# Optimization experiments

Hardware: AMD Instinct MI355X
Metric: run time of the kernel (lower is better)

Reference implementation:

```python
import jax, jax.numpy as jnp
import numpy as np

D = 384      # ViT-S feature dim (feat_dim_lookup['s'])
H = 6        # module forces num_heads = 6
L = 12       # ViT-S depth
RATIO = 0.1  # attention_mask_ratio
EPS = 1e-6


def layernorm(x, g, b):
    m = x.mean(-1, keepdims=True)
    v = ((x - m) ** 2).mean(-1, keepdims=True)
    return (x - m) * jax.lax.rsqrt(v + EPS) * g + b


def masked_attn(x, w_qkv, b_qkv, w_o, b_o):
    # Patch._fix_attn_masking: full softmax attention, threshold at ratio*row_max, renormalize.
    B, N, Dm = x.shape
    dh = Dm // H
    qkv = (x @ w_qkv + b_qkv).reshape(B, N, 3, H, dh)
    q = qkv[:, :, 0].transpose(0, 2, 1, 3)  # [B,H,N,dh]
    k = qkv[:, :, 1].transpose(0, 2, 1, 3)
    v = qkv[:, :, 2].transpose(0, 2, 1, 3)
    scores = jnp.einsum('bhqd,bhkd->bhqk', q, k) * (dh ** -0.5)
    attn = jax.nn.softmax(scores, axis=-1)
    thresh = RATIO * attn.max(axis=-1, keepdims=True)
    attn = jnp.where(attn >= thresh, attn, 0.0)
    attn = attn / attn.sum(axis=-1, keepdims=True)  # re-normalize
    out = jnp.einsum('bhqk,bhkd->bhqd', attn, v)
    out = out.transpose(0, 2, 1, 3).reshape(B, N, Dm)
    return out @ w_o + b_o, attn


def block(x, p):
    w_qkv, b_qkv, w_o, b_o, g1, be1, g2, be2, w1, b1, w2, b2 = p
    h, attn = masked_attn(layernorm(x, g1, be1), w_qkv, b_qkv, w_o, b_o)
    x = x + h
    h = layernorm(x, g2, be2) @ w1 + b1
    h = jax.nn.gelu(h, approximate=False) @ w2 + b2
    return x + h, attn


def setup_inputs() -> dict:
    key = jax.random.key(0)
    ks = jax.random.split(key, 8)
    B, N = 2, 962  # 2 transforms; (1+(160-8)//5)**2 + 1 cls = 962 tokens
    s = 0.02
    return {
        'x': jax.random.normal(ks[0], (B, N, D), jnp.float32),
        'w_qkv': jax.random.normal(ks[1], (L, D, 3 * D), jnp.float32) * s,
        'b_qkv': jnp.zeros((L, 3 * D), jnp.float32),
        'w_proj': jax.random.normal(ks[2], (L, D, D), jnp.float32) * s,
        'b_proj': jnp.zeros((L, D), jnp.float32),
        'ln1_g': jnp.ones((L, D), jnp.float32),
        'ln1_b': jnp.zeros((L, D), jnp.float32),
        'ln2_g': jnp.ones((L, D), jnp.float32),
        'ln2_b': jnp.zeros((L, D), jnp.float32),
        'w_fc1': jax.random.normal(ks[3], (L, D, 4 * D), jnp.float32) * s,
        'b_fc1': jnp.zeros((L, 4 * D), jnp.float32),
        'w_fc2': jax.random.normal(ks[4], (L, 4 * D, D), jnp.float32) * s,
        'b_fc2': jnp.zeros((L, D), jnp.float32),
        'lnf_g': jnp.ones((D,), jnp.float32),
        'lnf_b': jnp.zeros((D,), jnp.float32),
    }


def reference(x, w_qkv, b_qkv, w_proj, b_proj, ln1_g, ln1_b, ln2_g, ln2_b,
              w_fc1, b_fc1, w_fc2, b_fc2, lnf_g, lnf_b):
    params = (w_qkv, b_qkv, w_proj, b_proj, ln1_g, ln1_b, ln2_g, ln2_b,
              w_fc1, b_fc1, w_fc2, b_fc2)
    first = jax.tree_util.tree_map(lambda a: a[:-1], params)
    last = jax.tree_util.tree_map(lambda a: a[-1], params)

    def scan_fn(h, p):
        h, _ = block(h, p)
        return h, None

    x, _ = jax.lax.scan(scan_fn, x, first)  # blocks 0..L-2
    x, attn = block(x, last)                # last block, keep masked attention
    feats = layernorm(x, lnf_g, lnf_b)      # [B, N, D]
    return feats, attn
```

## Files before the change

kernel.cpp:

```cpp
#include <hip/hip_runtime.h>
#include <hip/hip_bf16.h>
#include <math.h>

typedef __bf16 bf16_t;
typedef __bf16 bf16x8 __attribute__((ext_vector_type(8)));
typedef float f32x4 __attribute__((ext_vector_type(4)));

#define NEGBIG -3.0e38f

__global__ void __launch_bounds__(256) tr_k(
    const float* __restrict__ W, bf16_t* __restrict__ Wt, int K, int N)
{
    __shared__ float T[32][33];
    const size_t per = (size_t)K * N;
    const float* Wl = W + blockIdx.z * per;
    bf16_t* Wtl = Wt + blockIdx.z * per;
    int n0 = blockIdx.x * 32, k0 = blockIdx.y * 32;
    int tx = threadIdx.x & 31, ty = threadIdx.x >> 5;
#pragma unroll
    for (int i = 0; i < 4; ++i)
        T[ty + 8 * i][tx] = Wl[(size_t)(k0 + ty + 8 * i) * N + n0 + tx];
    __syncthreads();
#pragma unroll
    for (int i = 0; i < 4; ++i)
        Wtl[(size_t)(n0 + ty + 8 * i) * K + k0 + tx] = (bf16_t)T[tx][ty + 8 * i];
}

template <int MODE>
__global__ void __launch_bounds__(256) gemm_k(
    const bf16_t* __restrict__ A, const bf16_t* __restrict__ Bt,
    const float* __restrict__ bias, int M, int N, int K,
    bf16_t* __restrict__ outb,
    bf16_t* __restrict__ qb, bf16_t* __restrict__ kb, bf16_t* __restrict__ vtb)
{
    __shared__ alignas(16) bf16_t As[2][64][72];
    __shared__ alignas(16) bf16_t Bs[2][64][72];

    const int tid  = threadIdx.x;
    const int wave = tid >> 6, lane = tid & 63;
    const int m0 = blockIdx.y * 64, n0 = blockIdx.x * 64;
    const int rb = (wave >> 1) * 32, cb = (wave & 1) * 32;
    const int q4 = lane >> 4, mm = lane & 15;

    const int lrow = tid >> 3;
    const int lcol = (tid & 7) * 8;

    const bf16_t* pA0 = A  + (size_t)(m0 + lrow) * K + lcol;
    const bf16_t* pA1 = pA0 + (size_t)32 * K;
    const bf16_t* pB0 = Bt + (size_t)(n0 + lrow) * K + lcol;
    const bf16_t* pB1 = pB0 + (size_t)32 * K;

    f32x4 acc[2][2] = {};
    bf16x8 va0, va1, vb0, vb1;

    va0 = *(const bf16x8*)(pA0);
    va1 = *(const bf16x8*)(pA1);
    vb0 = *(const bf16x8*)(pB0);
    vb1 = *(const bf16x8*)(pB1);
    *(bf16x8*)(&As[0][lrow][lcol])      = va0;
    *(bf16x8*)(&As[0][lrow + 32][lcol]) = va1;
    *(bf16x8*)(&Bs[0][lrow][lcol])      = vb0;
    *(bf16x8*)(&Bs[0][lrow + 32][lcol]) = vb1;

    int cur = 0;
    for (int k0 = 0; k0 < K; k0 += 64) {
        __syncthreads();
        const bool has_next = (k0 + 64 < K);
        if (has_next) {
            va0 = *(const bf16x8*)(pA0 + k0 + 64);
            va1 = *(const bf16x8*)(pA1 + k0 + 64);
            vb0 = *(const bf16x8*)(pB0 + k0 + 64);
            vb1 = *(const bf16x8*)(pB1 + k0 + 64);
        }
#pragma unroll
        for (int kc = 0; kc < 64; kc += 32) {
            bf16x8 a0 = *(const bf16x8*)(&As[cur][rb + mm][kc + q4 * 8]);
            bf16x8 a1 = *(const bf16x8*)(&As[cur][rb + 16 + mm][kc + q4 * 8]);
            bf16x8 b0 = *(const bf16x8*)(&Bs[cur][cb + mm][kc + q4 * 8]);
            bf16x8 b1 = *(const bf16x8*)(&Bs[cur][cb + 16 + mm][kc + q4 * 8]);
            acc[0][0] = __builtin_amdgcn_mfma_f32_16x16x32_bf16(a0, b0, acc[0][0], 0, 0, 0);
            acc[0][1] = __builtin_amdgcn_mfma_f32_16x16x32_bf16(a0, b1, acc[0][1], 0, 0, 0);
            acc[1][0] = __builtin_amdgcn_mfma_f32_16x16x32_bf16(a1, b0, acc[1][0], 0, 0, 0);
            acc[1][1] = __builtin_amdgcn_mfma_f32_16x16x32_bf16(a1, b1, acc[1][1], 0, 0, 0);
        }
        if (has_next) {
            int nxt = cur ^ 1;
            *(bf16x8*)(&As[nxt][lrow][lcol])      = va0;
            *(bf16x8*)(&As[nxt][lrow + 32][lcol]) = va1;
            *(bf16x8*)(&Bs[nxt][lrow][lcol])      = vb0;
            *(bf16x8*)(&Bs[nxt][lrow + 32][lcol]) = vb1;
            cur = nxt;
        }
    }

#pragma unroll
    for (int i = 0; i < 2; ++i)
#pragma unroll
    for (int j = 0; j < 2; ++j) {
        int gc = n0 + cb + j * 16 + mm;
        float bv = bias[gc];
#pragma unroll
        for (int r = 0; r < 4; ++r) {
            int gr = m0 + rb + i * 16 + q4 * 4 + r;
            if (gr >= M) continue;
            float val = acc[i][j][r] + bv;
            if (MODE == 2) {
                float g = 0.5f * val * (1.0f + erff(val * 0.70710678118654752f));
                outb[(size_t)gr * N + gc] = (bf16_t)g;
            } else {
                int which = gc / 384, rem = gc % 384;
                int h = rem >> 6, d = rem & 63;
                int b = gr / 962, n = gr % 962;
                int bh = b * 6 + h;
                bf16_t bvv = (bf16_t)val;
                if (which == 0)      qb[((size_t)bh * 962 + n) * 64 + d] = bvv;
                else if (which == 1) kb[((size_t)bh * 962 + n) * 64 + d] = bvv;
                else                 vtb[((size_t)bh * 64 + d) * 992 + n] = bvv;
            }
        }
    }
}

template <int KLEN>
__global__ void __launch_bounds__(256) gemm_sp(
    const bf16_t* __restrict__ A, int lda,
    const bf16_t* __restrict__ Bt, int ldb,
    const float* __restrict__ bias, int M, int N,
    float* __restrict__ resid)
{
    __shared__ alignas(16) bf16_t As[2][64][72];
    __shared__ alignas(16) bf16_t Bs[2][64][72];

    const int tid  = threadIdx.x;
    const int wave = tid >> 6, lane = tid & 63;
    const int m0 = blockIdx.y * 64, n0 = blockIdx.x * 64;
    const int rb = (wave >> 1) * 32, cb = (wave & 1) * 32;
    const int q4 = lane >> 4, mm = lane & 15;
    const int ks = blockIdx.z * KLEN;

    const int lrow = tid >> 3;
    const int lcol = (tid & 7) * 8;

    const bf16_t* pA0 = A  + (size_t)(m0 + lrow) * lda + ks + lcol;
    const bf16_t* pA1 = pA0 + (size_t)32 * lda;
    const bf16_t* pB0 = Bt + (size_t)(n0 + lrow) * ldb + ks + lcol;
    const bf16_t* pB1 = pB0 + (size_t)32 * ldb;

    f32x4 acc[2][2] = {};
    bf16x8 va0, va1, vb0, vb1;

    va0 = *(const bf16x8*)(pA0);
    va1 = *(const bf16x8*)(pA1);
    vb0 = *(const bf16x8*)(pB0);
    vb1 = *(const bf16x8*)(pB1);
    *(bf16x8*)(&As[0][lrow][lcol])      = va0;
    *(bf16x8*)(&As[0][lrow + 32][lcol]) = va1;
    *(bf16x8*)(&Bs[0][lrow][lcol])      = vb0;
    *(bf16x8*)(&Bs[0][lrow + 32][lcol]) = vb1;

    int cur = 0;
    for (int k0 = 0; k0 < KLEN; k0 += 64) {
        __syncthreads();
        const bool has_next = (k0 + 64 < KLEN);
        if (has_next) {
            va0 = *(const bf16x8*)(pA0 + k0 + 64);
            va1 = *(const bf16x8*)(pA1 + k0 + 64);
            vb0 = *(const bf16x8*)(pB0 + k0 + 64);
            vb1 = *(const bf16x8*)(pB1 + k0 + 64);
        }
#pragma unroll
        for (int kc = 0; kc < 64; kc += 32) {
            bf16x8 a0 = *(const bf16x8*)(&As[cur][rb + mm][kc + q4 * 8]);
            bf16x8 a1 = *(const bf16x8*)(&As[cur][rb + 16 + mm][kc + q4 * 8]);
            bf16x8 b0 = *(const bf16x8*)(&Bs[cur][cb + mm][kc + q4 * 8]);
            bf16x8 b1 = *(const bf16x8*)(&Bs[cur][cb + 16 + mm][kc + q4 * 8]);
            acc[0][0] = __builtin_amdgcn_mfma_f32_16x16x32_bf16(a0, b0, acc[0][0], 0, 0, 0);
            acc[0][1] = __builtin_amdgcn_mfma_f32_16x16x32_bf16(a0, b1, acc[0][1], 0, 0, 0);
            acc[1][0] = __builtin_amdgcn_mfma_f32_16x16x32_bf16(a1, b0, acc[1][0], 0, 0, 0);
            acc[1][1] = __builtin_amdgcn_mfma_f32_16x16x32_bf16(a1, b1, acc[1][1], 0, 0, 0);
        }
        if (has_next) {
            int nxt = cur ^ 1;
            *(bf16x8*)(&As[nxt][lrow][lcol])      = va0;
            *(bf16x8*)(&As[nxt][lrow + 32][lcol]) = va1;
            *(bf16x8*)(&Bs[nxt][lrow][lcol])      = vb0;
            *(bf16x8*)(&Bs[nxt][lrow + 32][lcol]) = vb1;
            cur = nxt;
        }
    }

#pragma unroll
    for (int i = 0; i < 2; ++i)
#pragma unroll
    for (int j = 0; j < 2; ++j) {
        int gc = n0 + cb + j * 16 + mm;
        float bv = (blockIdx.z == 0) ? bias[gc] : 0.f;
#pragma unroll
        for (int r = 0; r < 4; ++r) {
            int gr = m0 + rb + i * 16 + q4 * 4 + r;
            if (gr >= M) continue;
            atomicAdd(&resid[(size_t)gr * N + gc], acc[i][j][r] + bv);
        }
    }
}

__global__ void __launch_bounds__(256) attn_k(
    const bf16_t* __restrict__ qb, const bf16_t* __restrict__ kb,
    const bf16_t* __restrict__ vtb, bf16_t* __restrict__ attnout,
    float* __restrict__ attn_save)
{
    __shared__ alignas(16) bf16_t S[16][1000];

    const int tid  = threadIdx.x;
    const int wave = tid >> 6, lane = tid & 63;
    const int q4 = lane >> 4, mm = lane & 15;
    const int bh = blockIdx.y, qt = blockIdx.x;
    const int qrow0 = qt * 16;

    int qr = qrow0 + mm; if (qr > 961) qr = 961;
    const bf16_t* qptr = qb + ((size_t)bh * 962 + qr) * 64 + q4 * 8;
    bf16x8 aq0 = *(const bf16x8*)(qptr);
    bf16x8 aq1 = *(const bf16x8*)(qptr + 32);

    for (int ct = wave; ct < 61; ct += 4) {
        int kr = ct * 16 + mm; if (kr > 961) kr = 961;
        const bf16_t* kptr = kb + ((size_t)bh * 962 + kr) * 64 + q4 * 8;
        bf16x8 b0 = *(const bf16x8*)(kptr);
        bf16x8 b1 = *(const bf16x8*)(kptr + 32);
        f32x4 acc = {};
        acc = __builtin_amdgcn_mfma_f32_16x16x32_bf16(aq0, b0, acc, 0, 0, 0);
        acc = __builtin_amdgcn_mfma_f32_16x16x32_bf16(aq1, b1, acc, 0, 0, 0);
        int col = ct * 16 + mm;
#pragma unroll
        for (int r = 0; r < 4; ++r) {
            int row = q4 * 4 + r;
            if (col < 962) S[row][col] = (bf16_t)(acc[r] * 0.125f);
        }
    }
    for (int idx = tid; idx < 16 * 38; idx += 256) {
        int r = idx / 38, c = 962 + idx % 38;
        S[r][c] = (bf16_t)NEGBIG;
    }
    __syncthreads();

    const int trow = tid >> 4, ti = tid & 15;
    float e[8][8];
    float mx = NEGBIG;
#pragma unroll
    for (int t = 0; t < 8; ++t) {
        int c8 = ti * 8 + 128 * t;
        bf16x8 xv;
        if (c8 < 1000) xv = *(const bf16x8*)(&S[trow][c8]);
        else {
#pragma unroll
            for (int j = 0; j < 8; ++j) xv[j] = (bf16_t)NEGBIG;
        }
#pragma unroll
        for (int j = 0; j < 8; ++j) { e[t][j] = (float)xv[j]; mx = fmaxf(mx, e[t][j]); }
    }
#pragma unroll
    for (int off = 8; off > 0; off >>= 1) mx = fmaxf(mx, __shfl_xor(mx, off, 16));

    float sum = 0.f;
#pragma unroll
    for (int t = 0; t < 8; ++t)
#pragma unroll
    for (int j = 0; j < 8; ++j) {
        float ev = __expf(e[t][j] - mx);
        e[t][j] = ev;
        if (ev >= 0.1f) sum += ev;
    }
#pragma unroll
    for (int off = 8; off > 0; off >>= 1) sum += __shfl_xor(sum, off, 16);
    float inv = 1.0f / sum;

    int row_g = qrow0 + trow;
#pragma unroll
    for (int t = 0; t < 8; ++t) {
        int c8 = ti * 8 + 128 * t;
        if (c8 >= 1000) continue;
        bf16x8 pv;
#pragma unroll
        for (int j = 0; j < 8; ++j) {
            float pp = (e[t][j] >= 0.1f) ? e[t][j] * inv : 0.f;
            e[t][j] = pp;
            pv[j] = (bf16_t)pp;
        }
        *(bf16x8*)(&S[trow][c8]) = pv;
        if (attn_save && row_g < 962) {
#pragma unroll
            for (int j = 0; j < 8; ++j)
                if (c8 + j < 962)
                    attn_save[((size_t)bh * 962 + row_g) * 962 + c8 + j] = e[t][j];
        }
    }
    __syncthreads();

    const int wc0 = wave * 16;
    f32x4 o = {};
    for (int kc = 0; kc < 31; ++kc) {
        bf16x8 pa = *(const bf16x8*)(&S[mm][kc * 32 + q4 * 8]);
        bf16x8 vb = *(const bf16x8*)(vtb + ((size_t)bh * 64 + wc0 + mm) * 992 + kc * 32 + q4 * 8);
        o = __builtin_amdgcn_mfma_f32_16x16x32_bf16(pa, vb, o, 0, 0, 0);
    }
    int b = bh / 6, h = bh % 6;
#pragma unroll
    for (int r = 0; r < 4; ++r) {
        int qrr = qrow0 + q4 * 4 + r;
        if (qrr < 962)
            attnout[((size_t)(b * 962 + qrr)) * 384 + h * 64 + wc0 + mm] = (bf16_t)o[r];
    }
}

template <typename OT>
__global__ void __launch_bounds__(256) ln_k(
    const float* __restrict__ x, const float* __restrict__ g,
    const float* __restrict__ b, OT* __restrict__ out)
{
    int t = blockIdx.x * 4 + (threadIdx.x >> 6);
    int lane = threadIdx.x & 63;
    const float* xp = x + (size_t)t * 384;
    float v[6];
    float s = 0.f;
#pragma unroll
    for (int i = 0; i < 6; ++i) { v[i] = xp[lane + 64 * i]; s += v[i]; }
    for (int off = 32; off > 0; off >>= 1) s += __shfl_xor(s, off);
    float mean = s * (1.0f / 384.0f);
    float s2 = 0.f;
#pragma unroll
    for (int i = 0; i < 6; ++i) { float d = v[i] - mean; s2 += d * d; }
    for (int off = 32; off > 0; off >>= 1) s2 += __shfl_xor(s2, off);
    float rstd = rsqrtf(s2 * (1.0f / 384.0f) + 1e-6f);
#pragma unroll
    for (int i = 0; i < 6; ++i) {
        int c = lane + 64 * i;
        float y = (v[i] - mean) * rstd * g[c] + b[c];
        out[(size_t)t * 384 + c] = (OT)y;
    }
}

extern "C" void kernel_launch(void* const* d_in, const int* in_sizes, int n_in,
                              void* d_out, int out_size, void* d_ws, size_t ws_size,
                              hipStream_t stream)
{
    const float* xin    = (const float*)d_in[0];
    const float* w_qkv  = (const float*)d_in[1];
    const float* b_qkv  = (const float*)d_in[2];
    const float* w_proj = (const float*)d_in[3];
    const float* b_proj = (const float*)d_in[4];
    const float* ln1g   = (const float*)d_in[5];
    const float* ln1b   = (const float*)d_in[6];
    const float* ln2g   = (const float*)d_in[7];
    const float* ln2b   = (const float*)d_in[8];
    const float* w_fc1  = (const float*)d_in[9];
    const float* b_fc1  = (const float*)d_in[10];
    const float* w_fc2  = (const float*)d_in[11];
    const float* b_fc2  = (const float*)d_in[12];
    const float* lnfg   = (const float*)d_in[13];
    const float* lnfb   = (const float*)d_in[14];

    float* feats     = (float*)d_out;
    float* attn_save = feats + 738816;

    char* p = (char*)d_ws;
    auto alloc = [&](size_t bytes) {
        char* r = p;
        p += (bytes + 255) & ~(size_t)255;
        return r;
    };
    float*  x_f32   = (float*)alloc(1924ull * 384 * 4);
    bf16_t* xn      = (bf16_t*)alloc(1984ull * 384 * 2);
    bf16_t* qbuf    = (bf16_t*)alloc(12ull * 962 * 64 * 2);
    bf16_t* kbuf    = (bf16_t*)alloc(12ull * 962 * 64 * 2);
    bf16_t* vtbuf   = (bf16_t*)alloc(12ull * 64 * 992 * 2);
    bf16_t* attnout = (bf16_t*)alloc(1984ull * 384 * 2);
    bf16_t* mlp1    = (bf16_t*)alloc(1984ull * 1536 * 2);
    bf16_t* wt_qkv  = (bf16_t*)alloc(12ull * 1152 * 384 * 2);
    bf16_t* wt_proj = (bf16_t*)alloc(12ull * 384 * 384 * 2);
    bf16_t* wt_fc1  = (bf16_t*)alloc(12ull * 1536 * 384 * 2);
    bf16_t* wt_fc2  = (bf16_t*)alloc(12ull * 384 * 1536 * 2);

    tr_k<<<dim3(36, 12, 12), dim3(256), 0, stream>>>(w_qkv,  wt_qkv,  384, 1152);
    tr_k<<<dim3(12, 12, 12), dim3(256), 0, stream>>>(w_proj, wt_proj, 384, 384);
    tr_k<<<dim3(48, 12, 12), dim3(256), 0, stream>>>(w_fc1,  wt_fc1,  384, 1536);
    tr_k<<<dim3(12, 48, 12), dim3(256), 0, stream>>>(w_fc2,  wt_fc2,  1536, 384);

    hipMemcpyAsync(x_f32, xin, 738816ull * 4, hipMemcpyDeviceToDevice, stream);

    for (int l = 0; l < 12; ++l) {
        ln_k<bf16_t><<<dim3(481), dim3(256), 0, stream>>>(x_f32, ln1g + l * 384, ln1b + l * 384, xn);
        gemm_k<0><<<dim3(18, 31), dim3(256), 0, stream>>>(
            xn, wt_qkv + (size_t)l * 1152 * 384, b_qkv + l * 1152,
            1924, 1152, 384, nullptr, qbuf, kbuf, vtbuf);
        attn_k<<<dim3(61, 12), dim3(256), 0, stream>>>(
            qbuf, kbuf, vtbuf, attnout, (l == 11) ? attn_save : (float*)nullptr);
        gemm_sp<192><<<dim3(6, 31, 2), dim3(256), 0, stream>>>(
            attnout, 384, wt_proj + (size_t)l * 384 * 384, 384, b_proj + l * 384,
            1924, 384, x_f32);
        ln_k<bf16_t><<<dim3(481), dim3(256), 0, stream>>>(x_f32, ln2g + l * 384, ln2b + l * 384, xn);
        gemm_k<2><<<dim3(24, 31), dim3(256), 0, stream>>>(
            xn, wt_fc1 + (size_t)l * 1536 * 384, b_fc1 + l * 1536,
            1924, 1536, 384, mlp1, nullptr, nullptr, nullptr);
        gemm_sp<384><<<dim3(6, 31, 4), dim3(256), 0, stream>>>(
            mlp1, 1536, wt_fc2 + (size_t)l * 384 * 1536, 1536, b_fc2 + l * 384,
            1924, 384, x_f32);
    }
    ln_k<float><<<dim3(481), dim3(256), 0, stream>>>(x_f32, lnfg, lnfb, feats);
}
```

Measured before the change: 1.062 ms.

## Use direct global-to-LDS loads with XOR swizzle, merge transpose launches, add MFMA priority

```diff
diff --git a/kernel.cpp b/kernel.cpp
--- a/kernel.cpp
+++ b/kernel.cpp
@@ -8,14 +8,74 @@
 
 #define NEGBIG -3.0e38f
 
-__global__ void __launch_bounds__(256) tr_k(
-    const float* __restrict__ W, bf16_t* __restrict__ Wt, int K, int N)
+__device__ __forceinline__ void gload16(const void* g, void* l) {
+    __builtin_amdgcn_global_load_lds(
+        (const __attribute__((address_space(1))) void*)g,
+        (__attribute__((address_space(3))) void*)l, 16, 0, 0);
+}
+
+struct GemmSM { bf16_t As[2][64][64]; bf16_t Bs[2][64][64]; };
+
+__device__ __forceinline__ void gemm_core(
+    GemmSM* sg, const bf16_t* A, int lda, const bf16_t* Bt, int ldb, int K,
+    f32x4 acc[2][2])
+{
+    const int tid  = threadIdx.x;
+    const int wave = tid >> 6, lane = tid & 63;
+    const int rb = (wave >> 1) * 32, cb = (wave & 1) * 32;
+    const int q4 = lane >> 4, mm = lane & 15;
+    const int sw = (mm & 7) << 3;
+
+    const int sr   = lane >> 3;
+    const int scol = ((lane & 7) ^ sr) << 3;
+    const bf16_t* gA0 = A  + (size_t)(8 * wave + sr) * lda + scol;
+    const bf16_t* gA1 = gA0 + (size_t)32 * lda;
+    const bf16_t* gB0 = Bt + (size_t)(8 * wave + sr) * ldb + scol;
+    const bf16_t* gB1 = gB0 + (size_t)32 * ldb;
+
+    auto stage = [&](int buf, int k) {
+        gload16(gA0 + k, &sg->As[buf][8 * wave][0]);
+        gload16(gA1 + k, &sg->As[buf][8 * wave + 32][0]);
+        gload16(gB0 + k, &sg->Bs[buf][8 * wave][0]);
+        gload16(gB1 + k, &sg->Bs[buf][8 * wave + 32][0]);
+    };
+
+    stage(0, 0);
+    int cur = 0;
+    for (int k0 = 0; k0 < K; k0 += 64) {
+        __syncthreads();
+        if (k0 + 64 < K) stage(cur ^ 1, k0 + 64);
+#pragma unroll
+        for (int kc = 0; kc < 64; kc += 32) {
+            bf16x8 a0 = *(const bf16x8*)(&sg->As[cur][rb + mm][(kc + q4 * 8) ^ sw]);
+            bf16x8 a1 = *(const bf16x8*)(&sg->As[cur][rb + 16 + mm][(kc + q4 * 8) ^ sw]);
+            bf16x8 b0 = *(const bf16x8*)(&sg->Bs[cur][cb + mm][(kc + q4 * 8) ^ sw]);
+            bf16x8 b1 = *(const bf16x8*)(&sg->Bs[cur][cb + 16 + mm][(kc + q4 * 8) ^ sw]);
+            acc[0][0] = __builtin_amdgcn_mfma_f32_16x16x32_bf16(a0, b0, acc[0][0], 0, 0, 0);
+            acc[0][1] = __builtin_amdgcn_mfma_f32_16x16x32_bf16(a0, b1, acc[0][1], 0, 0, 0);
+            acc[1][0] = __builtin_amdgcn_mfma_f32_16x16x32_bf16(a1, b0, acc[1][0], 0, 0, 0);
+            acc[1][1] = __builtin_amdgcn_mfma_f32_16x16x32_bf16(a1, b1, acc[1][1], 0, 0, 0);
+        }
+        cur ^= 1;
+    }
+}
+
+__global__ void __launch_bounds__(256) trall_k(
+    const float* __restrict__ w_qkv, const float* __restrict__ w_proj,
+    const float* __restrict__ w_fc1, const float* __restrict__ w_fc2,
+    bf16_t* __restrict__ wt_qkv, bf16_t* __restrict__ wt_proj,
+    bf16_t* __restrict__ wt_fc1, bf16_t* __restrict__ wt_fc2)
 {
     __shared__ float T[32][33];
-    const size_t per = (size_t)K * N;
-    const float* Wl = W + blockIdx.z * per;
-    bf16_t* Wtl = Wt + blockIdx.z * per;
-    int n0 = blockIdx.x * 32, k0 = blockIdx.y * 32;
+    int t = blockIdx.x;
+    int z = t / 1728, r = t % 1728;
+    const float* W; bf16_t* Wt; int K, N, n0, k0;
+    if (r < 432)       { W = w_qkv;  Wt = wt_qkv;  K = 384;  N = 1152; n0 = (r % 36) * 32;               k0 = (r / 36) * 32; }
+    else if (r < 576)  { W = w_proj; Wt = wt_proj; K = 384;  N = 384;  int rr = r - 432;  n0 = (rr % 12) * 32; k0 = (rr / 12) * 32; }
+    else if (r < 1152) { W = w_fc1;  Wt = wt_fc1;  K = 384;  N = 1536; int rr = r - 576;  n0 = (rr % 48) * 32; k0 = (rr / 48) * 32; }
+    else               { W = w_fc2;  Wt = wt_fc2;  K = 1536; N = 384;  int rr = r - 1152; n0 = (rr % 12) * 32; k0 = (rr / 12) * 32; }
+    const float* Wl = W + (size_t)z * K * N;
+    bf16_t* Wtl = Wt + (size_t)z * K * N;
     int tx = threadIdx.x & 31, ty = threadIdx.x >> 5;
 #pragma unroll
     for (int i = 0; i < 4; ++i)
@@ -33,66 +93,14 @@
     bf16_t* __restrict__ outb,
     bf16_t* __restrict__ qb, bf16_t* __restrict__ kb, bf16_t* __restrict__ vtb)
 {
-    __shared__ alignas(16) bf16_t As[2][64][72];
-    __shared__ alignas(16) bf16_t Bs[2][64][72];
-
-    const int tid  = threadIdx.x;
+    __shared__ GemmSM sm;
+    const int tid = threadIdx.x;
     const int wave = tid >> 6, lane = tid & 63;
     const int m0 = blockIdx.y * 64, n0 = blockIdx.x * 64;
     const int rb = (wave >> 1) * 32, cb = (wave & 1) * 32;
     const int q4 = lane >> 4, mm = lane & 15;
-
-    const int lrow = tid >> 3;
-    const int lcol = (tid & 7) * 8;
-
-    const bf16_t* pA0 = A  + (size_t)(m0 + lrow) * K + lcol;
-    const bf16_t* pA1 = pA0 + (size_t)32 * K;
-    const bf16_t* pB0 = Bt + (size_t)(n0 + lrow) * K + lcol;
-    const bf16_t* pB1 = pB0 + (size_t)32 * K;
-
     f32x4 acc[2][2] = {};
-    bf16x8 va0, va1, vb0, vb1;
-
-    va0 = *(const bf16x8*)(pA0);
-    va1 = *(const bf16x8*)(pA1);
-    vb0 = *(const bf16x8*)(pB0);
-    vb1 = *(const bf16x8*)(pB1);
-    *(bf16x8*)(&As[0][lrow][lcol])      = va0;
-    *(bf16x8*)(&As[0][lrow + 32][lcol]) = va1;
-    *(bf16x8*)(&Bs[0][lrow][lcol])      = vb0;
-    *(bf16x8*)(&Bs[0][lrow + 32][lcol]) = vb1;
-
-    int cur = 0;
-    for (int k0 = 0; k0 < K; k0 += 64) {
-        __syncthreads();
-        const bool has_next = (k0 + 64 < K);
-        if (has_next) {
-            va0 = *(const bf16x8*)(pA0 + k0 + 64);
-            va1 = *(const bf16x8*)(pA1 + k0 + 64);
-            vb0 = *(const bf16x8*)(pB0 + k0 + 64);
-            vb1 = *(const bf16x8*)(pB1 + k0 + 64);
-        }
-#pragma unroll
-        for (int kc = 0; kc < 64; kc += 32) {
-            bf16x8 a0 = *(const bf16x8*)(&As[cur][rb + mm][kc + q4 * 8]);
-            bf16x8 a1 = *(const bf16x8*)(&As[cur][rb + 16 + mm][kc + q4 * 8]);
-            bf16x8 b0 = *(const bf16x8*)(&Bs[cur][cb + mm][kc + q4 * 8]);
-            bf16x8 b1 = *(const bf16x8*)(&Bs[cur][cb + 16 + mm][kc + q4 * 8]);
-            acc[0][0] = __builtin_amdgcn_mfma_f32_16x16x32_bf16(a0, b0, acc[0][0], 0, 0, 0);
-            acc[0][1] = __builtin_amdgcn_mfma_f32_16x16x32_bf16(a0, b1, acc[0][1], 0, 0, 0);
-            acc[1][0] = __builtin_amdgcn_mfma_f32_16x16x32_bf16(a1, b0, acc[1][0], 0, 0, 0);
-            acc[1][1] = __builtin_amdgcn_mfma_f32_16x16x32_bf16(a1, b1, acc[1][1], 0, 0, 0);
-        }
-        if (has_next) {
-            int nxt = cur ^ 1;
-            *(bf16x8*)(&As[nxt][lrow][lcol])      = va0;
-            *(bf16x8*)(&As[nxt][lrow + 32][lcol]) = va1;
-            *(bf16x8*)(&Bs[nxt][lrow][lcol])      = vb0;
-            *(bf16x8*)(&Bs[nxt][lrow + 32][lcol]) = vb1;
-            cur = nxt;
-        }
-    }
-
+    gemm_core(&sm, A + (size_t)m0 * K, K, Bt + (size_t)n0 * K, K, K, acc);
 #pragma unroll
     for (int i = 0; i < 2; ++i)
 #pragma unroll
@@ -128,67 +136,15 @@
     const float* __restrict__ bias, int M, int N,
     float* __restrict__ resid)
 {
-    __shared__ alignas(16) bf16_t As[2][64][72];
-    __shared__ alignas(16) bf16_t Bs[2][64][72];
-
-    const int tid  = threadIdx.x;
+    __shared__ GemmSM sm;
+    const int tid = threadIdx.x;
     const int wave = tid >> 6, lane = tid & 63;
     const int m0 = blockIdx.y * 64, n0 = blockIdx.x * 64;
     const int rb = (wave >> 1) * 32, cb = (wave & 1) * 32;
     const int q4 = lane >> 4, mm = lane & 15;
     const int ks = blockIdx.z * KLEN;
-
-    const int lrow = tid >> 3;
-    const int lcol = (tid & 7) * 8;
-
-    const bf16_t* pA0 = A  + (size_t)(m0 + lrow) * lda + ks + lcol;
-    const bf16_t* pA1 = pA0 + (size_t)32 * lda;
-    const bf16_t* pB0 = Bt + (size_t)(n0 + lrow) * ldb + ks + lcol;
-    const bf16_t* pB1 = pB0 + (size_t)32 * ldb;
-
     f32x4 acc[2][2] = {};
-    bf16x8 va0, va1, vb0, vb1;
-
-    va0 = *(const bf16x8*)(pA0);
-    va1 = *(const bf16x8*)(pA1);
-    vb0 = *(const bf16x8*)(pB0);
-    vb1 = *(const bf16x8*)(pB1);
-    *(bf16x8*)(&As[0][lrow][lcol])      = va0;
-    *(bf16x8*)(&As[0][lrow + 32][lcol]) = va1;
-    *(bf16x8*)(&Bs[0][lrow][lcol])      = vb0;
-    *(bf16x8*)(&Bs[0][lrow + 32][lcol]) = vb1;
-
-    int cur = 0;
-    for (int k0 = 0; k0 < KLEN; k0 += 64) {
-        __syncthreads();
-        const bool has_next = (k0 + 64 < KLEN);
-        if (has_next) {
-            va0 = *(const bf16x8*)(pA0 + k0 + 64);
-            va1 = *(const bf16x8*)(pA1 + k0 + 64);
-            vb0 = *(const bf16x8*)(pB0 + k0 + 64);
-            vb1 = *(const bf16x8*)(pB1 + k0 + 64);
-        }
-#pragma unroll
-        for (int kc = 0; kc < 64; kc += 32) {
-            bf16x8 a0 = *(const bf16x8*)(&As[cur][rb + mm][kc + q4 * 8]);
-            bf16x8 a1 = *(const bf16x8*)(&As[cur][rb + 16 + mm][kc + q4 * 8]);
-            bf16x8 b0 = *(const bf16x8*)(&Bs[cur][cb + mm][kc + q4 * 8]);
-            bf16x8 b1 = *(const bf16x8*)(&Bs[cur][cb + 16 + mm][kc + q4 * 8]);
-            acc[0][0] = __builtin_amdgcn_mfma_f32_16x16x32_bf16(a0, b0, acc[0][0], 0, 0, 0);
-            acc[0][1] = __builtin_amdgcn_mfma_f32_16x16x32_bf16(a0, b1, acc[0][1], 0, 0, 0);
-            acc[1][0] = __builtin_amdgcn_mfma_f32_16x16x32_bf16(a1, b0, acc[1][0], 0, 0, 0);
-            acc[1][1] = __builtin_amdgcn_mfma_f32_16x16x32_bf16(a1, b1, acc[1][1], 0, 0, 0);
-        }
-        if (has_next) {
-            int nxt = cur ^ 1;
-            *(bf16x8*)(&As[nxt][lrow][lcol])      = va0;
-            *(bf16x8*)(&As[nxt][lrow + 32][lcol]) = va1;
-            *(bf16x8*)(&Bs[nxt][lrow][lcol])      = vb0;
-            *(bf16x8*)(&Bs[nxt][lrow + 32][lcol]) = vb1;
-            cur = nxt;
-        }
-    }
-
+    gemm_core(&sm, A + (size_t)m0 * lda + ks, lda, Bt + (size_t)n0 * ldb + ks, ldb, KLEN, acc);
 #pragma unroll
     for (int i = 0; i < 2; ++i)
 #pragma unroll
@@ -228,8 +184,10 @@
         bf16x8 b0 = *(const bf16x8*)(kptr);
         bf16x8 b1 = *(const bf16x8*)(kptr + 32);
         f32x4 acc = {};
+        __builtin_amdgcn_s_setprio(1);
         acc = __builtin_amdgcn_mfma_f32_16x16x32_bf16(aq0, b0, acc, 0, 0, 0);
         acc = __builtin_amdgcn_mfma_f32_16x16x32_bf16(aq1, b1, acc, 0, 0, 0);
+        __builtin_amdgcn_s_setprio(0);
         int col = ct * 16 + mm;
 #pragma unroll
         for (int r = 0; r < 4; ++r) {
@@ -301,7 +259,9 @@
     for (int kc = 0; kc < 31; ++kc) {
         bf16x8 pa = *(const bf16x8*)(&S[mm][kc * 32 + q4 * 8]);
         bf16x8 vb = *(const bf16x8*)(vtb + ((size_t)bh * 64 + wc0 + mm) * 992 + kc * 32 + q4 * 8);
+        __builtin_amdgcn_s_setprio(1);
         o = __builtin_amdgcn_mfma_f32_16x16x32_bf16(pa, vb, o, 0, 0, 0);
+        __builtin_amdgcn_s_setprio(0);
     }
     int b = bh / 6, h = bh % 6;
 #pragma unroll
@@ -380,10 +340,8 @@
     bf16_t* wt_fc1  = (bf16_t*)alloc(12ull * 1536 * 384 * 2);
     bf16_t* wt_fc2  = (bf16_t*)alloc(12ull * 384 * 1536 * 2);
 
-    tr_k<<<dim3(36, 12, 12), dim3(256), 0, stream>>>(w_qkv,  wt_qkv,  384, 1152);
-    tr_k<<<dim3(12, 12, 12), dim3(256), 0, stream>>>(w_proj, wt_proj, 384, 384);
-    tr_k<<<dim3(48, 12, 12), dim3(256), 0, stream>>>(w_fc1,  wt_fc1,  384, 1536);
-    tr_k<<<dim3(12, 48, 12), dim3(256), 0, stream>>>(w_fc2,  wt_fc2,  1536, 384);
+    trall_k<<<dim3(20736), dim3(256), 0, stream>>>(
+        w_qkv, w_proj, w_fc1, w_fc2, wt_qkv, wt_proj, wt_fc1, wt_fc2);
 
     hipMemcpyAsync(x_f32, xin, 738816ull * 4, hipMemcpyDeviceToDevice, stream);
 
```

Measured after the change: 1.095 ms. 1.03x slower.
